# Optimization experiments

Measured on AMD Instinct MI355X. Metric: run time of the kernel, lower is better.

## Reference

```python
import jax, jax.numpy as jnp
import numpy as np

CODEBOOK_SIZE = 256
EMBED_DIM = 32
N_TOKENS = 524288
EPS = 1e-6


def l2norm(t, eps=EPS):
    # F.normalize(p=2): x / max(||x||, eps)
    n = jnp.sqrt(jnp.sum(t * t, axis=-1, keepdims=True))
    return t / jnp.maximum(n, eps)


def setup_inputs() -> dict:
    key = jax.random.key(0)
    kx, kw = jax.random.split(key)
    x = jax.random.normal(kx, (N_TOKENS, EMBED_DIM), dtype=jnp.float32)
    # embedding.weight.data.uniform_(-1/codebook_size, 1/codebook_size)
    codebook = jax.random.uniform(
        kw, (CODEBOOK_SIZE, EMBED_DIM), dtype=jnp.float32,
        minval=-1.0 / CODEBOOK_SIZE, maxval=1.0 / CODEBOOK_SIZE)
    return {"x": x, "codebook": codebook}


def reference(x, codebook):
    # --- find_nearest_codes: cdist + argmin + gather ---
    # squared euclidean distances have the same argmin as torch.cdist
    x2 = jnp.sum(x * x, axis=-1, keepdims=True)            # [N, 1]
    c2 = jnp.sum(codebook * codebook, axis=-1)             # [K]
    d2 = x2 - 2.0 * (x @ codebook.T) + c2[None, :]         # [N, K]
    indices = jnp.argmin(d2, axis=1)                       # [N] int
    quantized = codebook[indices]                          # [N, D]

    # --- update_usage: histogram over codes ---
    counts = jnp.zeros((CODEBOOK_SIZE,), dtype=jnp.float32).at[indices].add(1.0)

    # --- rotate_to(x, quantized): rotation-trick gradient estimator ---
    u = jax.lax.stop_gradient(l2norm(x))                   # detached direction of src
    q = jax.lax.stop_gradient(l2norm(quantized))           # detached direction of tgt
    w = jax.lax.stop_gradient(l2norm(u + q))               # Householder bisector, detached
    e = x                                                  # gradient flows through e only
    ew = jnp.sum(e * w, axis=-1, keepdims=True)            # (e @ w_col)
    eu = jnp.sum(e * u, axis=-1, keepdims=True)            # (e @ u_col)
    rotated = e - 2.0 * ew * w + 2.0 * eu * q              # [N, D]

    return rotated, indices, counts
```

## Files before the change

kernel.cpp:

```cpp
#include <hip/hip_runtime.h>

#define N_TOK   524288
#define KC      256
#define D       32
#define EPSF    1e-6f
#define TPT     64
#define NTILES  (N_TOK / TPT)
#define NBLK    768
#define BLKT    256

__global__ __launch_bounds__(BLKT) void vq_main(
    const float* __restrict__ x, const float* __restrict__ cb,
    float* __restrict__ out_rot, float* __restrict__ out_idx,
    float* __restrict__ ws_hist, float* __restrict__ out_cnt, int use_ws)
{
    __shared__ float ct[D][KC];
    __shared__ float c2s[KC];
    __shared__ float xt[D][TPT];
    __shared__ float x2s[TPT];
    __shared__ int   bidx[TPT];
    __shared__ float hist[KC];

    const int tid = threadIdx.x;

    {
#pragma clang fp contract(off)
        const float4* cb4 = (const float4*)(cb + (size_t)tid * D);
        float4 r[8];
#pragma unroll
        for (int j = 0; j < 8; j++) r[j] = cb4[j];
        float t[32];
#pragma unroll
        for (int j = 0; j < 8; j++) {
            t[4 * j + 0] = r[j].x * r[j].x;
            t[4 * j + 1] = r[j].y * r[j].y;
            t[4 * j + 2] = r[j].z * r[j].z;
            t[4 * j + 3] = r[j].w * r[j].w;
        }
        float pr[8];
#pragma unroll
        for (int j = 0; j < 8; j++)
            pr[j] = ((t[j] + t[j + 8]) + t[j + 16]) + t[j + 24];
        c2s[tid] = ((pr[0] + pr[1]) + (pr[2] + pr[3])) + ((pr[4] + pr[5]) + (pr[6] + pr[7]));
#pragma unroll
        for (int j = 0; j < 8; j++) {
            ct[4 * j + 0][tid] = r[j].x;
            ct[4 * j + 1][tid] = r[j].y;
            ct[4 * j + 2][tid] = r[j].z;
            ct[4 * j + 3][tid] = r[j].w;
        }
        hist[tid] = 0.f;
    }
    const int tt = tid >> 4;
    const int tc = tid & 15;
    __syncthreads();

    for (int tile = blockIdx.x; tile < NTILES; tile += gridDim.x) {
        const int tok0 = tile * TPT;

        {
            const float4* xg = (const float4*)(x + (size_t)tok0 * D + (size_t)tid * 8);
            float4 a = xg[0], b = xg[1];
            int tok = tid >> 2;
            int k0  = (tid & 3) * 8;
            xt[k0 + 0][tok] = a.x; xt[k0 + 1][tok] = a.y;
            xt[k0 + 2][tok] = a.z; xt[k0 + 3][tok] = a.w;
            xt[k0 + 4][tok] = b.x; xt[k0 + 5][tok] = b.y;
            xt[k0 + 6][tok] = b.z; xt[k0 + 7][tok] = b.w;
        }
        __syncthreads();

        if (tid < TPT) {
#pragma clang fp contract(off)
            float t[32];
#pragma unroll
            for (int k = 0; k < 32; k++) { float v = xt[k][tid]; t[k] = v * v; }
            float pr[8];
#pragma unroll
            for (int j = 0; j < 8; j++)
                pr[j] = ((t[j] + t[j + 8]) + t[j + 16]) + t[j + 24];
            x2s[tid] = ((pr[0] + pr[1]) + (pr[2] + pr[3])) + ((pr[4] + pr[5]) + (pr[6] + pr[7]));
        }
        __syncthreads();

        float x4[4];
#pragma unroll
        for (int i = 0; i < 4; i++) x4[i] = x2s[tt * 4 + i];

        float bestv[4] = {3.4e38f, 3.4e38f, 3.4e38f, 3.4e38f};
        int   besti[4] = {0x7fffffff, 0x7fffffff, 0x7fffffff, 0x7fffffff};
#pragma unroll
        for (int chunk = 0; chunk < 2; chunk++) {
            const int cbase = chunk * 128 + tc * 8;
            float acc[4][8];
#pragma unroll
            for (int i = 0; i < 4; i++)
#pragma unroll
                for (int j = 0; j < 8; j++) acc[i][j] = 0.f;

#pragma unroll 8
            for (int k = 0; k < D; k++) {
                const float4 xv = *(const float4*)&xt[k][tt * 4];
                const float4 c0 = *(const float4*)&ct[k][cbase];
                const float4 c1 = *(const float4*)&ct[k][cbase + 4];
                const float xs[4] = {xv.x, xv.y, xv.z, xv.w};
                const float cs[8] = {c0.x, c0.y, c0.z, c0.w, c1.x, c1.y, c1.z, c1.w};
#pragma unroll
                for (int i = 0; i < 4; i++)
#pragma unroll
                    for (int j = 0; j < 8; j++)
                        acc[i][j] = __builtin_fmaf(xs[i], cs[j], acc[i][j]);
            }
#pragma unroll
            for (int j = 0; j < 8; j++) {
                const float c2v = c2s[cbase + j];
#pragma unroll
                for (int i = 0; i < 4; i++) {
                    float t2 = x4[i] - 2.0f * acc[i][j];
                    float s  = t2 + c2v;
                    if (s < bestv[i]) { bestv[i] = s; besti[i] = cbase + j; }
                }
            }
        }
#pragma unroll
        for (int m = 1; m < 16; m <<= 1) {
#pragma unroll
            for (int i = 0; i < 4; i++) {
                float ov = __shfl_xor(bestv[i], m, 64);
                int   oi = __shfl_xor(besti[i], m, 64);
                if (ov < bestv[i] || (ov == bestv[i] && oi < besti[i])) {
                    bestv[i] = ov; besti[i] = oi;
                }
            }
        }
        if (tc == 0) {
#pragma unroll
            for (int i = 0; i < 4; i++) bidx[tt * 4 + i] = besti[i];
        }
        __syncthreads();

        {
            const int tok = tid >> 2;
            const int sub = tid & 3;
            const size_t gtok = (size_t)tok0 + tok;
            const float4* xg = (const float4*)(x + gtok * D + sub * 8);
            float4 xa = xg[0], xb = xg[1];
            const int bi = bidx[tok];
            const float4* cg = (const float4*)(cb + (size_t)bi * D + sub * 8);
            float4 ca = cg[0], cbv = cg[1];

            float xs8[8] = {xa.x, xa.y, xa.z, xa.w, xb.x, xb.y, xb.z, xb.w};
            float cs8[8] = {ca.x, ca.y, ca.z, ca.w, cbv.x, cbv.y, cbv.z, cbv.w};

            float px2 = 0.f, pc2 = 0.f;
#pragma unroll
            for (int j = 0; j < 8; j++) { px2 = fmaf(xs8[j], xs8[j], px2); pc2 = fmaf(cs8[j], cs8[j], pc2); }
            float x2 = px2 + __shfl_xor(px2, 1, 64); x2 += __shfl_xor(x2, 2, 64);
            float c2 = pc2 + __shfl_xor(pc2, 1, 64); c2 += __shfl_xor(c2, 2, 64);
            const float inx = 1.f / fmaxf(sqrtf(x2), EPSF);
            const float inc = 1.f / fmaxf(sqrtf(c2), EPSF);

            float us8[8], qs8[8], ws8[8];
            float pw2 = 0.f;
#pragma unroll
            for (int j = 0; j < 8; j++) {
                us8[j] = xs8[j] * inx;
                qs8[j] = cs8[j] * inc;
                ws8[j] = us8[j] + qs8[j];
                pw2 = fmaf(ws8[j], ws8[j], pw2);
            }
            float w2 = pw2 + __shfl_xor(pw2, 1, 64); w2 += __shfl_xor(w2, 2, 64);
            const float inw = 1.f / fmaxf(sqrtf(w2), EPSF);

            float pew = 0.f, peu = 0.f;
#pragma unroll
            for (int j = 0; j < 8; j++) {
                ws8[j] *= inw;
                pew = fmaf(xs8[j], ws8[j], pew);
                peu = fmaf(xs8[j], us8[j], peu);
            }
            float ew = pew + __shfl_xor(pew, 1, 64); ew += __shfl_xor(ew, 2, 64);
            float eu = peu + __shfl_xor(peu, 1, 64); eu += __shfl_xor(eu, 2, 64);

            float ro[8];
#pragma unroll
            for (int j = 0; j < 8; j++)
                ro[j] = xs8[j] - 2.f * ew * ws8[j] + 2.f * eu * qs8[j];

            float4* og = (float4*)(out_rot + gtok * D + sub * 8);
            og[0] = make_float4(ro[0], ro[1], ro[2], ro[3]);
            og[1] = make_float4(ro[4], ro[5], ro[6], ro[7]);

            if (sub == 0) {
                out_idx[gtok] = (float)bi;
                atomicAdd(&hist[bi], 1.f);
            }
        }
        __syncthreads();
    }

    if (use_ws) ws_hist[(size_t)blockIdx.x * KC + tid] = hist[tid];
    else        atomicAdd(&out_cnt[tid], hist[tid]);
}

__global__ __launch_bounds__(256) void vq_reduce(const float* __restrict__ ws,
                                                 float* __restrict__ out_cnt)
{
    const int c = blockIdx.x * 8 + (threadIdx.x >> 5);
    const int l = threadIdx.x & 31;
    float s = 0.f;
    for (int b = l; b < NBLK; b += 32) s += ws[(size_t)b * KC + c];
#pragma unroll
    for (int m = 1; m < 32; m <<= 1) s += __shfl_xor(s, m, 64);
    if (l == 0) out_cnt[c] = s;
}

extern "C" void kernel_launch(void* const* d_in, const int* in_sizes, int n_in,
                              void* d_out, int out_size, void* d_ws, size_t ws_size,
                              hipStream_t stream)
{
    const float* x  = (const float*)d_in[0];
    const float* cb = (const float*)d_in[1];
    float* out      = (float*)d_out;
    float* out_rot  = out;
    float* out_idx  = out + (size_t)N_TOK * D;
    float* out_cnt  = out_idx + N_TOK;

    const size_t ws_need = (size_t)NBLK * KC * sizeof(float);
    const int use_ws = (ws_size >= ws_need) ? 1 : 0;
    if (!use_ws) hipMemsetAsync(out_cnt, 0, KC * sizeof(float), stream);

    vq_main<<<NBLK, BLKT, 0, stream>>>(x, cb, out_rot, out_idx,
                                       (float*)d_ws, out_cnt, use_ws);
    if (use_ws) vq_reduce<<<32, 256, 0, stream>>>((const float*)d_ws, out_cnt);
}
```

Before: 242.1 us.

## Double-buffer token tiles, prefetch next tile, and keep x in registers

Prefetches the next tile's x into registers and stages it into a second shared buffer, so per-tile barriers drop from four to one. The squared norm of x is now computed with cross-lane shuffles during staging. The x values are reused from registers in the rotation phase instead of being reloaded from global memory. Best indices are passed by wave shuffle rather than through shared memory. It also computes all 16 codes per thread in one pass with an XOR-swizzled x layout, which raises register pressure in exchange for fewer LDS x reads and fewer barriers.

```diff
diff --git a/kernel.cpp b/kernel.cpp
--- a/kernel.cpp
+++ b/kernel.cpp
@@ -16,12 +16,12 @@
 {
     __shared__ float ct[D][KC];
     __shared__ float c2s[KC];
-    __shared__ float xt[D][TPT];
-    __shared__ float x2s[TPT];
-    __shared__ int   bidx[TPT];
+    __shared__ float xt[2][D][TPT];
+    __shared__ float x2s[2][TPT];
     __shared__ float hist[KC];
 
-    const int tid = threadIdx.x;
+    const int tid  = threadIdx.x;
+    const int lane = tid & 63;
 
     {
 #pragma clang fp contract(off)
@@ -51,77 +51,95 @@
         }
         hist[tid] = 0.f;
     }
-    const int tt = tid >> 4;
-    const int tc = tid & 15;
+
+    const int tt   = tid >> 4;
+    const int tc   = tid & 15;
+    const int tok  = tid >> 2;
+    const int sub  = tid & 3;
+    const int colw = tok ^ (sub << 4);
+
+    auto stage = [&](int buf, float4 a, float4 b) {
+#pragma clang fp contract(off)
+        float xs[8] = {a.x, a.y, a.z, a.w, b.x, b.y, b.z, b.w};
+        const int k0 = sub * 8;
+#pragma unroll
+        for (int j = 0; j < 8; j++) xt[buf][k0 + j][colw] = xs[j];
+        float sq[8];
+#pragma unroll
+        for (int j = 0; j < 8; j++) sq[j] = xs[j] * xs[j];
+        const int base = lane & ~3;
+        float pr[8];
+#pragma unroll
+        for (int j = 0; j < 8; j++) {
+            float t01 = sq[j] + __shfl_xor(sq[j], 1, 64);
+            float s2  = __shfl(sq[j], base + 2, 64);
+            float s3  = __shfl(sq[j], base + 3, 64);
+            pr[j] = (t01 + s2) + s3;
+        }
+        float v = ((pr[0] + pr[1]) + (pr[2] + pr[3])) + ((pr[4] + pr[5]) + (pr[6] + pr[7]));
+        if (sub == 0) x2s[buf][tok] = v;
+    };
+
+    float4 aC, bC;
+    {
+        const float4* xg = (const float4*)(x + (size_t)blockIdx.x * TPT * D + (size_t)tid * 8);
+        aC = xg[0]; bC = xg[1];
+    }
+    stage(0, aC, bC);
     __syncthreads();
 
+    int cur = 0;
     for (int tile = blockIdx.x; tile < NTILES; tile += gridDim.x) {
-        const int tok0 = tile * TPT;
-
-        {
-            const float4* xg = (const float4*)(x + (size_t)tok0 * D + (size_t)tid * 8);
-            float4 a = xg[0], b = xg[1];
-            int tok = tid >> 2;
-            int k0  = (tid & 3) * 8;
-            xt[k0 + 0][tok] = a.x; xt[k0 + 1][tok] = a.y;
-            xt[k0 + 2][tok] = a.z; xt[k0 + 3][tok] = a.w;
-            xt[k0 + 4][tok] = b.x; xt[k0 + 5][tok] = b.y;
-            xt[k0 + 6][tok] = b.z; xt[k0 + 7][tok] = b.w;
-        }
-        __syncthreads();
-
-        if (tid < TPT) {
-#pragma clang fp contract(off)
-            float t[32];
-#pragma unroll
-            for (int k = 0; k < 32; k++) { float v = xt[k][tid]; t[k] = v * v; }
-            float pr[8];
-#pragma unroll
-            for (int j = 0; j < 8; j++)
-                pr[j] = ((t[j] + t[j + 8]) + t[j + 16]) + t[j + 24];
-            x2s[tid] = ((pr[0] + pr[1]) + (pr[2] + pr[3])) + ((pr[4] + pr[5]) + (pr[6] + pr[7]));
-        }
-        __syncthreads();
+        const int nt = tile + gridDim.x;
+        const bool hasN = (nt < NTILES);
+        float4 aN = aC, bN = bC;
+        if (hasN) {
+            const float4* xg = (const float4*)(x + (size_t)nt * TPT * D + (size_t)tid * 8);
+            aN = xg[0]; bN = xg[1];
+        }
 
         float x4[4];
 #pragma unroll
-        for (int i = 0; i < 4; i++) x4[i] = x2s[tt * 4 + i];
+        for (int i = 0; i < 4; i++) x4[i] = x2s[cur][tt * 4 + i];
+
+        float acc[4][16];
+#pragma unroll
+        for (int i = 0; i < 4; i++)
+#pragma unroll
+            for (int j = 0; j < 16; j++) acc[i][j] = 0.f;
+
+#pragma unroll 4
+        for (int k = 0; k < D; k++) {
+            const int xcol = (tt * 4) ^ ((k >> 3) << 4);
+            const float4 xv = *(const float4*)&xt[cur][k][xcol];
+            const float4 v0 = *(const float4*)&ct[k][tc * 4];
+            const float4 v1 = *(const float4*)&ct[k][64 + tc * 4];
+            const float4 v2 = *(const float4*)&ct[k][128 + tc * 4];
+            const float4 v3 = *(const float4*)&ct[k][192 + tc * 4];
+            const float xs[4]  = {xv.x, xv.y, xv.z, xv.w};
+            const float cs[16] = {v0.x, v0.y, v0.z, v0.w, v1.x, v1.y, v1.z, v1.w,
+                                  v2.x, v2.y, v2.z, v2.w, v3.x, v3.y, v3.z, v3.w};
+#pragma unroll
+            for (int i = 0; i < 4; i++)
+#pragma unroll
+                for (int j = 0; j < 16; j++)
+                    acc[i][j] = __builtin_fmaf(xs[i], cs[j], acc[i][j]);
+        }
 
         float bestv[4] = {3.4e38f, 3.4e38f, 3.4e38f, 3.4e38f};
         int   besti[4] = {0x7fffffff, 0x7fffffff, 0x7fffffff, 0x7fffffff};
 #pragma unroll
-        for (int chunk = 0; chunk < 2; chunk++) {
-            const int cbase = chunk * 128 + tc * 8;
-            float acc[4][8];
-#pragma unroll
-            for (int i = 0; i < 4; i++)
-#pragma unroll
-                for (int j = 0; j < 8; j++) acc[i][j] = 0.f;
-
-#pragma unroll 8
-            for (int k = 0; k < D; k++) {
-                const float4 xv = *(const float4*)&xt[k][tt * 4];
-                const float4 c0 = *(const float4*)&ct[k][cbase];
-                const float4 c1 = *(const float4*)&ct[k][cbase + 4];
-                const float xs[4] = {xv.x, xv.y, xv.z, xv.w};
-                const float cs[8] = {c0.x, c0.y, c0.z, c0.w, c1.x, c1.y, c1.z, c1.w};
-#pragma unroll
-                for (int i = 0; i < 4; i++)
-#pragma unroll
-                    for (int j = 0; j < 8; j++)
-                        acc[i][j] = __builtin_fmaf(xs[i], cs[j], acc[i][j]);
-            }
-#pragma unroll
-            for (int j = 0; j < 8; j++) {
-                const float c2v = c2s[cbase + j];
-#pragma unroll
-                for (int i = 0; i < 4; i++) {
-                    float t2 = x4[i] - 2.0f * acc[i][j];
-                    float s  = t2 + c2v;
-                    if (s < bestv[i]) { bestv[i] = s; besti[i] = cbase + j; }
-                }
-            }
-        }
+        for (int j = 0; j < 16; j++) {
+            const int code = (j >> 2) * 64 + tc * 4 + (j & 3);
+            const float c2v = c2s[code];
+#pragma unroll
+            for (int i = 0; i < 4; i++) {
+                float t2 = x4[i] - 2.0f * acc[i][j];
+                float s  = t2 + c2v;
+                if (s < bestv[i]) { bestv[i] = s; besti[i] = code; }
+            }
+        }
+
 #pragma unroll
         for (int m = 1; m < 16; m <<= 1) {
 #pragma unroll
@@ -133,23 +151,21 @@
                 }
             }
         }
-        if (tc == 0) {
-#pragma unroll
-            for (int i = 0; i < 4; i++) bidx[tt * 4 + i] = besti[i];
-        }
-        __syncthreads();
+
+        const int src = lane & 48;
+        const int b0 = __shfl(besti[0], src, 64);
+        const int b1 = __shfl(besti[1], src, 64);
+        const int b2 = __shfl(besti[2], src, 64);
+        const int b3 = __shfl(besti[3], src, 64);
+        const int ii = (lane >> 2) & 3;
+        const int bi = (ii == 0) ? b0 : (ii == 1) ? b1 : (ii == 2) ? b2 : b3;
 
         {
-            const int tok = tid >> 2;
-            const int sub = tid & 3;
-            const size_t gtok = (size_t)tok0 + tok;
-            const float4* xg = (const float4*)(x + gtok * D + sub * 8);
-            float4 xa = xg[0], xb = xg[1];
-            const int bi = bidx[tok];
+            const size_t gtok = (size_t)tile * TPT + tok;
             const float4* cg = (const float4*)(cb + (size_t)bi * D + sub * 8);
             float4 ca = cg[0], cbv = cg[1];
 
-            float xs8[8] = {xa.x, xa.y, xa.z, xa.w, xb.x, xb.y, xb.z, xb.w};
+            float xs8[8] = {aC.x, aC.y, aC.z, aC.w, bC.x, bC.y, bC.z, bC.w};
             float cs8[8] = {ca.x, ca.y, ca.z, ca.w, cbv.x, cbv.y, cbv.z, cbv.w};
 
             float px2 = 0.f, pc2 = 0.f;
@@ -196,7 +212,10 @@
                 atomicAdd(&hist[bi], 1.f);
             }
         }
+
+        if (hasN) stage(cur ^ 1, aN, bN);
         __syncthreads();
+        aC = aN; bC = bN; cur ^= 1;
     }
 
     if (use_ws) ws_hist[(size_t)blockIdx.x * KC + tid] = hist[tid];
```

New measurement: 244.8 us. No clear change (+1.1%).

## Switch to one token per thread with codebook reads from global/scalar loads

Applied to the files above, without the earlier changes.

Replaces the shared-memory register-tiled 4x8 distance computation with a one-token-per-thread scheme. Each thread keeps its 32-element x row in registers and loops over all 256 codes, reading codebook rows directly from global memory through uniform, cache-resident loads. It also removes the persistent tile loop, launching one block per 256 tokens, and drops the shuffle reductions in the rotation epilogue. In exchange it loses the register-level reuse of the tiled GEMM, since each codebook element is now used once per load rather than across four tokens. Per-thread strided x loads of 128 bytes also coalesce less well.

```diff
diff --git a/kernel.cpp b/kernel.cpp
--- a/kernel.cpp
+++ b/kernel.cpp
@@ -4,21 +4,15 @@
 #define KC      256
 #define D       32
 #define EPSF    1e-6f
-#define TPT     64
-#define NTILES  (N_TOK / TPT)
-#define NBLK    768
+#define NBLK    2048
 #define BLKT    256
 
-__global__ __launch_bounds__(BLKT) void vq_main(
+__global__ __launch_bounds__(BLKT, 4) void vq_main(
     const float* __restrict__ x, const float* __restrict__ cb,
     float* __restrict__ out_rot, float* __restrict__ out_idx,
     float* __restrict__ ws_hist, float* __restrict__ out_cnt, int use_ws)
 {
-    __shared__ float ct[D][KC];
     __shared__ float c2s[KC];
-    __shared__ float xt[D][TPT];
-    __shared__ float x2s[TPT];
-    __shared__ int   bidx[TPT];
     __shared__ float hist[KC];
 
     const int tid = threadIdx.x;
@@ -42,162 +36,113 @@
         for (int j = 0; j < 8; j++)
             pr[j] = ((t[j] + t[j + 8]) + t[j + 16]) + t[j + 24];
         c2s[tid] = ((pr[0] + pr[1]) + (pr[2] + pr[3])) + ((pr[4] + pr[5]) + (pr[6] + pr[7]));
+        hist[tid] = 0.f;
+    }
+    __syncthreads();
+
+    const size_t tok = (size_t)blockIdx.x * BLKT + tid;
+
+    float xr[32];
+    {
+        const float4* xg = (const float4*)(x + tok * D);
 #pragma unroll
         for (int j = 0; j < 8; j++) {
-            ct[4 * j + 0][tid] = r[j].x;
-            ct[4 * j + 1][tid] = r[j].y;
-            ct[4 * j + 2][tid] = r[j].z;
-            ct[4 * j + 3][tid] = r[j].w;
+            float4 v = xg[j];
+            xr[4 * j + 0] = v.x; xr[4 * j + 1] = v.y;
+            xr[4 * j + 2] = v.z; xr[4 * j + 3] = v.w;
         }
-        hist[tid] = 0.f;
     }
-    const int tt = tid >> 4;
-    const int tc = tid & 15;
+
+    float x2v;
+    {
+#pragma clang fp contract(off)
+        float t[32];
+#pragma unroll
+        for (int k = 0; k < 32; k++) t[k] = xr[k] * xr[k];
+        float pr[8];
+#pragma unroll
+        for (int j = 0; j < 8; j++)
+            pr[j] = ((t[j] + t[j + 8]) + t[j + 16]) + t[j + 24];
+        x2v = ((pr[0] + pr[1]) + (pr[2] + pr[3])) + ((pr[4] + pr[5]) + (pr[6] + pr[7]));
+    }
+
+    float bestv = 3.4e38f;
+    int   besti = 0x7fffffff;
+#pragma unroll 2
+    for (int c = 0; c < KC; ++c) {
+        const float4* cr = (const float4*)(cb + (size_t)c * D);
+        const float4 q0 = cr[0], q1 = cr[1], q2 = cr[2], q3 = cr[3];
+        const float4 q4 = cr[4], q5 = cr[5], q6 = cr[6], q7 = cr[7];
+        const float cs[32] = {q0.x, q0.y, q0.z, q0.w, q1.x, q1.y, q1.z, q1.w,
+                              q2.x, q2.y, q2.z, q2.w, q3.x, q3.y, q3.z, q3.w,
+                              q4.x, q4.y, q4.z, q4.w, q5.x, q5.y, q5.z, q5.w,
+                              q6.x, q6.y, q6.z, q6.w, q7.x, q7.y, q7.z, q7.w};
+        float acc = 0.f;
+#pragma unroll
+        for (int k = 0; k < 32; ++k) acc = __builtin_fmaf(xr[k], cs[k], acc);
+        const float t2 = x2v - 2.0f * acc;
+        const float s  = t2 + c2s[c];
+        if (s < bestv) { bestv = s; besti = c; }
+    }
+
+    float cs[32];
+    {
+        const float4* cg = (const float4*)(cb + (size_t)besti * D);
+#pragma unroll
+        for (int j = 0; j < 8; j++) {
+            float4 v = cg[j];
+            cs[4 * j + 0] = v.x; cs[4 * j + 1] = v.y;
+            cs[4 * j + 2] = v.z; cs[4 * j + 3] = v.w;
+        }
+    }
+
+    float px2 = 0.f, pc2 = 0.f;
+#pragma unroll
+    for (int j = 0; j < 32; j++) {
+        px2 = fmaf(xr[j], xr[j], px2);
+        pc2 = fmaf(cs[j], cs[j], pc2);
+    }
+    const float inx = 1.f / fmaxf(sqrtf(px2), EPSF);
+    const float inc = 1.f / fmaxf(sqrtf(pc2), EPSF);
+
+    float pw2 = 0.f;
+#pragma unroll
+    for (int j = 0; j < 32; j++) {
+        const float wj = xr[j] * inx + cs[j] * inc;
+        pw2 = fmaf(wj, wj, pw2);
+    }
+    const float inw = 1.f / fmaxf(sqrtf(pw2), EPSF);
+
+    float pew = 0.f, peu = 0.f;
+#pragma unroll
+    for (int j = 0; j < 32; j++) {
+        const float uj = xr[j] * inx;
+        const float wj = (uj + cs[j] * inc) * inw;
+        pew = fmaf(xr[j], wj, pew);
+        peu = fmaf(xr[j], uj, peu);
+    }
+    const float ew = pew, eu = peu;
+
+    {
+        float4* og = (float4*)(out_rot + tok * D);
+#pragma unroll
+        for (int j = 0; j < 8; j++) {
+            float r4[4];
+#pragma unroll
+            for (int e = 0; e < 4; e++) {
+                const int jj = 4 * j + e;
+                const float uj = xr[jj] * inx;
+                const float wj = (uj + cs[jj] * inc) * inw;
+                const float qj = cs[jj] * inc;
+                r4[e] = xr[jj] - 2.f * ew * wj + 2.f * eu * qj;
+            }
+            og[j] = make_float4(r4[0], r4[1], r4[2], r4[3]);
+        }
+    }
+
+    out_idx[tok] = (float)besti;
+    atomicAdd(&hist[besti], 1.f);
     __syncthreads();
-
-    for (int tile = blockIdx.x; tile < NTILES; tile += gridDim.x) {
-        const int tok0 = tile * TPT;
-
-        {
-            const float4* xg = (const float4*)(x + (size_t)tok0 * D + (size_t)tid * 8);
-            float4 a = xg[0], b = xg[1];
-            int tok = tid >> 2;
-            int k0  = (tid & 3) * 8;
-            xt[k0 + 0][tok] = a.x; xt[k0 + 1][tok] = a.y;
-            xt[k0 + 2][tok] = a.z; xt[k0 + 3][tok] = a.w;
-            xt[k0 + 4][tok] = b.x; xt[k0 + 5][tok] = b.y;
-            xt[k0 + 6][tok] = b.z; xt[k0 + 7][tok] = b.w;
-        }
-        __syncthreads();
-
-        if (tid < TPT) {
-#pragma clang fp contract(off)
-            float t[32];
-#pragma unroll
-            for (int k = 0; k < 32; k++) { float v = xt[k][tid]; t[k] = v * v; }
-            float pr[8];
-#pragma unroll
-            for (int j = 0; j < 8; j++)
-                pr[j] = ((t[j] + t[j + 8]) + t[j + 16]) + t[j + 24];
-            x2s[tid] = ((pr[0] + pr[1]) + (pr[2] + pr[3])) + ((pr[4] + pr[5]) + (pr[6] + pr[7]));
-        }
-        __syncthreads();
-
-        float x4[4];
-#pragma unroll
-        for (int i = 0; i < 4; i++) x4[i] = x2s[tt * 4 + i];
-
-        float bestv[4] = {3.4e38f, 3.4e38f, 3.4e38f, 3.4e38f};
-        int   besti[4] = {0x7fffffff, 0x7fffffff, 0x7fffffff, 0x7fffffff};
-#pragma unroll
-        for (int chunk = 0; chunk < 2; chunk++) {
-            const int cbase = chunk * 128 + tc * 8;
-            float acc[4][8];
-#pragma unroll
-            for (int i = 0; i < 4; i++)
-#pragma unroll
-                for (int j = 0; j < 8; j++) acc[i][j] = 0.f;
-
-#pragma unroll 8
-            for (int k = 0; k < D; k++) {
-                const float4 xv = *(const float4*)&xt[k][tt * 4];
-                const float4 c0 = *(const float4*)&ct[k][cbase];
-                const float4 c1 = *(const float4*)&ct[k][cbase + 4];
-                const float xs[4] = {xv.x, xv.y, xv.z, xv.w};
-                const float cs[8] = {c0.x, c0.y, c0.z, c0.w, c1.x, c1.y, c1.z, c1.w};
-#pragma unroll
-                for (int i = 0; i < 4; i++)
-#pragma unroll
-                    for (int j = 0; j < 8; j++)
-                        acc[i][j] = __builtin_fmaf(xs[i], cs[j], acc[i][j]);
-            }
-#pragma unroll
-            for (int j = 0; j < 8; j++) {
-                const float c2v = c2s[cbase + j];
-#pragma unroll
-                for (int i = 0; i < 4; i++) {
-                    float t2 = x4[i] - 2.0f * acc[i][j];
-                    float s  = t2 + c2v;
-                    if (s < bestv[i]) { bestv[i] = s; besti[i] = cbase + j; }
-                }
-            }
-        }
-#pragma unroll
-        for (int m = 1; m < 16; m <<= 1) {
-#pragma unroll
-            for (int i = 0; i < 4; i++) {
-                float ov = __shfl_xor(bestv[i], m, 64);
-                int   oi = __shfl_xor(besti[i], m, 64);
-                if (ov < bestv[i] || (ov == bestv[i] && oi < besti[i])) {
-                    bestv[i] = ov; besti[i] = oi;
-                }
-            }
-        }
-        if (tc == 0) {
-#pragma unroll
-            for (int i = 0; i < 4; i++) bidx[tt * 4 + i] = besti[i];
-        }
-        __syncthreads();
-
-        {
-            const int tok = tid >> 2;
-            const int sub = tid & 3;
-            const size_t gtok = (size_t)tok0 + tok;
-            const float4* xg = (const float4*)(x + gtok * D + sub * 8);
-            float4 xa = xg[0], xb = xg[1];
-            const int bi = bidx[tok];
-            const float4* cg = (const float4*)(cb + (size_t)bi * D + sub * 8);
-            float4 ca = cg[0], cbv = cg[1];
-
-            float xs8[8] = {xa.x, xa.y, xa.z, xa.w, xb.x, xb.y, xb.z, xb.w};
-            float cs8[8] = {ca.x, ca.y, ca.z, ca.w, cbv.x, cbv.y, cbv.z, cbv.w};
-
-            float px2 = 0.f, pc2 = 0.f;
-#pragma unroll
-            for (int j = 0; j < 8; j++) { px2 = fmaf(xs8[j], xs8[j], px2); pc2 = fmaf(cs8[j], cs8[j], pc2); }
-            float x2 = px2 + __shfl_xor(px2, 1, 64); x2 += __shfl_xor(x2, 2, 64);
-            float c2 = pc2 + __shfl_xor(pc2, 1, 64); c2 += __shfl_xor(c2, 2, 64);
-            const float inx = 1.f / fmaxf(sqrtf(x2), EPSF);
-            const float inc = 1.f / fmaxf(sqrtf(c2), EPSF);
-
-            float us8[8], qs8[8], ws8[8];
-            float pw2 = 0.f;
-#pragma unroll
-            for (int j = 0; j < 8; j++) {
-                us8[j] = xs8[j] * inx;
-                qs8[j] = cs8[j] * inc;
-                ws8[j] = us8[j] + qs8[j];
-                pw2 = fmaf(ws8[j], ws8[j], pw2);
-            }
-            float w2 = pw2 + __shfl_xor(pw2, 1, 64); w2 += __shfl_xor(w2, 2, 64);
-            const float inw = 1.f / fmaxf(sqrtf(w2), EPSF);
-
-            float pew = 0.f, peu = 0.f;
-#pragma unroll
-            for (int j = 0; j < 8; j++) {
-                ws8[j] *= inw;
-                pew = fmaf(xs8[j], ws8[j], pew);
-                peu = fmaf(xs8[j], us8[j], peu);
-            }
-            float ew = pew + __shfl_xor(pew, 1, 64); ew += __shfl_xor(ew, 2, 64);
-            float eu = peu + __shfl_xor(peu, 1, 64); eu += __shfl_xor(eu, 2, 64);
-
-            float ro[8];
-#pragma unroll
-            for (int j = 0; j < 8; j++)
-                ro[j] = xs8[j] - 2.f * ew * ws8[j] + 2.f * eu * qs8[j];
-
-            float4* og = (float4*)(out_rot + gtok * D + sub * 8);
-            og[0] = make_float4(ro[0], ro[1], ro[2], ro[3]);
-            og[1] = make_float4(ro[4], ro[5], ro[6], ro[7]);
-
-            if (sub == 0) {
-                out_idx[gtok] = (float)bi;
-                atomicAdd(&hist[bi], 1.f);
-            }
-        }
-        __syncthreads();
-    }
 
     if (use_ws) ws_hist[(size_t)blockIdx.x * KC + tid] = hist[tid];
     else        atomicAdd(&out_cnt[tid], hist[tid]);
```

After: 281.5 us. 16.3% more time.

## Compute distances with split-bf16 MFMA and exact fp32 rescoring of near-ties

Applied to the files above, without the earlier changes.

Replaces the fp32 FMA distance GEMM with MFMA 16x16x32 bf16 instructions, splitting x and the codebook into hi/lo bf16 parts and using three MFMAs to approximate fp32 precision. Candidates within a margin of the per-token minimum are rescored in exact fp32 to keep the argmin matching the reference. Work is reorganized per wave (16-token strips) with no block-level barriers inside the loop, and the grid grows to 1024 blocks. The risks are divergent rescoring cost and argmin mismatches if the margin is too small.

```diff
diff --git a/kernel.cpp b/kernel.cpp
--- a/kernel.cpp
+++ b/kernel.cpp
@@ -4,24 +4,42 @@
 #define KC      256
 #define D       32
 #define EPSF    1e-6f
-#define TPT     64
-#define NTILES  (N_TOK / TPT)
-#define NBLK    768
+#define NBLK    1024
 #define BLKT    256
+#define NWAVES  (NBLK * 4)
+#define NSTRIP  (N_TOK / 16)
+#define SPW     (NSTRIP / NWAVES)
+#define MARGIN  1e-3f
+#define BIGF    3.4e38f
+
+typedef __attribute__((ext_vector_type(8))) short short8;
+typedef __attribute__((ext_vector_type(4))) float f32x4;
+
+__device__ __forceinline__ unsigned short f32_to_bf16_rne(float f) {
+    unsigned int u = __float_as_uint(f);
+    unsigned int r = u + 0x7fffu + ((u >> 16) & 1u);
+    return (unsigned short)(r >> 16);
+}
+__device__ __forceinline__ float bf16_to_f32(unsigned short h) {
+    return __uint_as_float(((unsigned int)h) << 16);
+}
 
 __global__ __launch_bounds__(BLKT) void vq_main(
     const float* __restrict__ x, const float* __restrict__ cb,
     float* __restrict__ out_rot, float* __restrict__ out_idx,
     float* __restrict__ ws_hist, float* __restrict__ out_cnt, int use_ws)
 {
-    __shared__ float ct[D][KC];
+    __shared__ unsigned int cbh[KC][20];
+    __shared__ unsigned int cbl[KC][20];
     __shared__ float c2s[KC];
-    __shared__ float xt[D][TPT];
-    __shared__ float x2s[TPT];
-    __shared__ int   bidx[TPT];
     __shared__ float hist[KC];
-
-    const int tid = threadIdx.x;
+    __shared__ float xs[4][16][36];
+    __shared__ float x2w[4][16];
+    __shared__ int   win[4][16];
+
+    const int tid  = threadIdx.x;
+    const int lane = tid & 63;
+    const int w    = tid >> 6;
 
     {
 #pragma clang fp contract(off)
@@ -29,125 +47,158 @@
         float4 r[8];
 #pragma unroll
         for (int j = 0; j < 8; j++) r[j] = cb4[j];
+        float v[32];
+#pragma unroll
+        for (int j = 0; j < 8; j++) {
+            v[4*j+0] = r[j].x; v[4*j+1] = r[j].y; v[4*j+2] = r[j].z; v[4*j+3] = r[j].w;
+        }
         float t[32];
 #pragma unroll
-        for (int j = 0; j < 8; j++) {
-            t[4 * j + 0] = r[j].x * r[j].x;
-            t[4 * j + 1] = r[j].y * r[j].y;
-            t[4 * j + 2] = r[j].z * r[j].z;
-            t[4 * j + 3] = r[j].w * r[j].w;
-        }
+        for (int k = 0; k < 32; k++) t[k] = v[k] * v[k];
         float pr[8];
 #pragma unroll
         for (int j = 0; j < 8; j++)
             pr[j] = ((t[j] + t[j + 8]) + t[j + 16]) + t[j + 24];
         c2s[tid] = ((pr[0] + pr[1]) + (pr[2] + pr[3])) + ((pr[4] + pr[5]) + (pr[6] + pr[7]));
-#pragma unroll
-        for (int j = 0; j < 8; j++) {
-            ct[4 * j + 0][tid] = r[j].x;
-            ct[4 * j + 1][tid] = r[j].y;
-            ct[4 * j + 2][tid] = r[j].z;
-            ct[4 * j + 3][tid] = r[j].w;
+
+        unsigned int hp[16], lp[16];
+#pragma unroll
+        for (int q = 0; q < 16; q++) { hp[q] = 0u; lp[q] = 0u; }
+#pragma unroll
+        for (int j = 0; j < 32; j++) {
+            unsigned short h = f32_to_bf16_rne(v[j]);
+            float lo = v[j] - bf16_to_f32(h);
+            unsigned short l = f32_to_bf16_rne(lo);
+            hp[j >> 1] |= ((unsigned int)h) << (16 * (j & 1));
+            lp[j >> 1] |= ((unsigned int)l) << (16 * (j & 1));
+        }
+#pragma unroll
+        for (int q = 0; q < 4; q++) {
+            ((uint4*)&cbh[tid][0])[q] = make_uint4(hp[4*q], hp[4*q+1], hp[4*q+2], hp[4*q+3]);
+            ((uint4*)&cbl[tid][0])[q] = make_uint4(lp[4*q], lp[4*q+1], lp[4*q+2], lp[4*q+3]);
         }
         hist[tid] = 0.f;
     }
-    const int tt = tid >> 4;
-    const int tc = tid & 15;
     __syncthreads();
 
-    for (int tile = blockIdx.x; tile < NTILES; tile += gridDim.x) {
-        const int tok0 = tile * TPT;
-
+    const int col = lane & 15;
+    const int kc  = lane >> 4;
+
+    float c2r[16];
+#pragma unroll
+    for (int t = 0; t < 16; t++) c2r[t] = c2s[t * 16 + col];
+
+    const int gw = blockIdx.x * 4 + w;
+
+    for (int s = 0; s < SPW; ++s) {
+        const int strip = gw + NWAVES * s;
+        const int tb    = strip * 16;
+
+        const float* xp = x + (size_t)(tb + col) * D + kc * 8;
+        const float4 f0 = *(const float4*)xp;
+        const float4 f1 = *(const float4*)(xp + 4);
+        *(float4*)&xs[w][col][kc * 8]     = f0;
+        *(float4*)&xs[w][col][kc * 8 + 4] = f1;
+
+        short8 ah, al;
         {
-            const float4* xg = (const float4*)(x + (size_t)tok0 * D + (size_t)tid * 8);
-            float4 a = xg[0], b = xg[1];
-            int tok = tid >> 2;
-            int k0  = (tid & 3) * 8;
-            xt[k0 + 0][tok] = a.x; xt[k0 + 1][tok] = a.y;
-            xt[k0 + 2][tok] = a.z; xt[k0 + 3][tok] = a.w;
-            xt[k0 + 4][tok] = b.x; xt[k0 + 5][tok] = b.y;
-            xt[k0 + 6][tok] = b.z; xt[k0 + 7][tok] = b.w;
-        }
-        __syncthreads();
-
-        if (tid < TPT) {
+            float xf[8] = {f0.x, f0.y, f0.z, f0.w, f1.x, f1.y, f1.z, f1.w};
+#pragma unroll
+            for (int j = 0; j < 8; j++) {
+                unsigned short h = f32_to_bf16_rne(xf[j]);
+                float lo = xf[j] - bf16_to_f32(h);
+                ah[j] = (short)h;
+                al[j] = (short)f32_to_bf16_rne(lo);
+            }
+        }
+
+        {
 #pragma clang fp contract(off)
-            float t[32];
-#pragma unroll
-            for (int k = 0; k < 32; k++) { float v = xt[k][tid]; t[k] = v * v; }
+            const int tok4 = lane >> 2, sub = lane & 3, base = lane & ~3;
+            const float4 a = *(const float4*)&xs[w][tok4][sub * 8];
+            const float4 b = *(const float4*)&xs[w][tok4][sub * 8 + 4];
+            float sq[8] = {a.x*a.x, a.y*a.y, a.z*a.z, a.w*a.w,
+                           b.x*b.x, b.y*b.y, b.z*b.z, b.w*b.w};
             float pr[8];
 #pragma unroll
-            for (int j = 0; j < 8; j++)
-                pr[j] = ((t[j] + t[j + 8]) + t[j + 16]) + t[j + 24];
-            x2s[tid] = ((pr[0] + pr[1]) + (pr[2] + pr[3])) + ((pr[4] + pr[5]) + (pr[6] + pr[7]));
-        }
-        __syncthreads();
-
-        float x4[4];
-#pragma unroll
-        for (int i = 0; i < 4; i++) x4[i] = x2s[tt * 4 + i];
-
-        float bestv[4] = {3.4e38f, 3.4e38f, 3.4e38f, 3.4e38f};
-        int   besti[4] = {0x7fffffff, 0x7fffffff, 0x7fffffff, 0x7fffffff};
-#pragma unroll
-        for (int chunk = 0; chunk < 2; chunk++) {
-            const int cbase = chunk * 128 + tc * 8;
-            float acc[4][8];
-#pragma unroll
-            for (int i = 0; i < 4; i++)
-#pragma unroll
-                for (int j = 0; j < 8; j++) acc[i][j] = 0.f;
-
-#pragma unroll 8
-            for (int k = 0; k < D; k++) {
-                const float4 xv = *(const float4*)&xt[k][tt * 4];
-                const float4 c0 = *(const float4*)&ct[k][cbase];
-                const float4 c1 = *(const float4*)&ct[k][cbase + 4];
-                const float xs[4] = {xv.x, xv.y, xv.z, xv.w};
-                const float cs[8] = {c0.x, c0.y, c0.z, c0.w, c1.x, c1.y, c1.z, c1.w};
-#pragma unroll
-                for (int i = 0; i < 4; i++)
-#pragma unroll
-                    for (int j = 0; j < 8; j++)
-                        acc[i][j] = __builtin_fmaf(xs[i], cs[j], acc[i][j]);
-            }
-#pragma unroll
-            for (int j = 0; j < 8; j++) {
-                const float c2v = c2s[cbase + j];
-#pragma unroll
-                for (int i = 0; i < 4; i++) {
-                    float t2 = x4[i] - 2.0f * acc[i][j];
-                    float s  = t2 + c2v;
-                    if (s < bestv[i]) { bestv[i] = s; besti[i] = cbase + j; }
+            for (int j = 0; j < 8; j++) {
+                float t01 = sq[j] + __shfl_xor(sq[j], 1, 64);
+                float s2  = __shfl(sq[j], base + 2, 64);
+                float s3  = __shfl(sq[j], base + 3, 64);
+                pr[j] = (t01 + s2) + s3;
+            }
+            float v = ((pr[0]+pr[1]) + (pr[2]+pr[3])) + ((pr[4]+pr[5]) + (pr[6]+pr[7]));
+            if (sub == 0) x2w[w][tok4] = v;
+        }
+
+        float sarr[16][4];
+        float mn[4] = {BIGF, BIGF, BIGF, BIGF};
+#pragma unroll
+        for (int t = 0; t < 16; ++t) {
+            const int code = t * 16 + col;
+            const short8 bh = *(const short8*)&cbh[code][kc * 4];
+            const short8 bl = *(const short8*)&cbl[code][kc * 4];
+            f32x4 acc = {0.f, 0.f, 0.f, 0.f};
+            acc = __builtin_amdgcn_mfma_f32_16x16x32_bf16(al, bh, acc, 0, 0, 0);
+            acc = __builtin_amdgcn_mfma_f32_16x16x32_bf16(ah, bl, acc, 0, 0, 0);
+            acc = __builtin_amdgcn_mfma_f32_16x16x32_bf16(ah, bh, acc, 0, 0, 0);
+#pragma unroll
+            for (int r = 0; r < 4; ++r) {
+                const float sv = __builtin_fmaf(-2.f, acc[r], c2r[t]);
+                sarr[t][r] = sv;
+                mn[r] = fminf(mn[r], sv);
+            }
+        }
+#pragma unroll
+        for (int m = 1; m < 16; m <<= 1)
+#pragma unroll
+            for (int r = 0; r < 4; ++r)
+                mn[r] = fminf(mn[r], __shfl_xor(mn[r], m, 64));
+
+        float bE[4] = {BIGF, BIGF, BIGF, BIGF};
+        int   bI[4] = {0x7fffffff, 0x7fffffff, 0x7fffffff, 0x7fffffff};
+#pragma unroll
+        for (int t = 0; t < 16; ++t)
+#pragma unroll
+            for (int r = 0; r < 4; ++r)
+                if (sarr[t][r] <= mn[r] + MARGIN) {
+                    const int code = t * 16 + col;
+                    const int trow = kc * 4 + r;
+                    const float* crow = cb + (size_t)code * D;
+                    float acc = 0.f;
+#pragma unroll
+                    for (int q = 0; q < 8; ++q) {
+                        const float4 xq = *(const float4*)&xs[w][trow][q * 4];
+                        const float4 cq = *(const float4*)&crow[q * 4];
+                        acc = __builtin_fmaf(xq.x, cq.x, acc);
+                        acc = __builtin_fmaf(xq.y, cq.y, acc);
+                        acc = __builtin_fmaf(xq.z, cq.z, acc);
+                        acc = __builtin_fmaf(xq.w, cq.w, acc);
+                    }
+                    const float t2 = x2w[w][trow] - 2.0f * acc;
+                    const float d  = t2 + c2s[code];
+                    if (d < bE[r] || (d == bE[r] && code < bI[r])) { bE[r] = d; bI[r] = code; }
                 }
-            }
-        }
-#pragma unroll
-        for (int m = 1; m < 16; m <<= 1) {
-#pragma unroll
-            for (int i = 0; i < 4; i++) {
-                float ov = __shfl_xor(bestv[i], m, 64);
-                int   oi = __shfl_xor(besti[i], m, 64);
-                if (ov < bestv[i] || (ov == bestv[i] && oi < besti[i])) {
-                    bestv[i] = ov; besti[i] = oi;
-                }
-            }
-        }
-        if (tc == 0) {
-#pragma unroll
-            for (int i = 0; i < 4; i++) bidx[tt * 4 + i] = besti[i];
-        }
-        __syncthreads();
+#pragma unroll
+        for (int m = 1; m < 16; m <<= 1)
+#pragma unroll
+            for (int r = 0; r < 4; ++r) {
+                const float ov = __shfl_xor(bE[r], m, 64);
+                const int   oi = __shfl_xor(bI[r], m, 64);
+                if (ov < bE[r] || (ov == bE[r] && oi < bI[r])) { bE[r] = ov; bI[r] = oi; }
+            }
+        if (col == 0)
+#pragma unroll
+            for (int r = 0; r < 4; ++r) win[w][kc * 4 + r] = bI[r];
 
         {
-            const int tok = tid >> 2;
-            const int sub = tid & 3;
-            const size_t gtok = (size_t)tok0 + tok;
-            const float4* xg = (const float4*)(x + gtok * D + sub * 8);
-            float4 xa = xg[0], xb = xg[1];
-            const int bi = bidx[tok];
+            const int tok = lane >> 2, sub = lane & 3;
+            const size_t gtok = (size_t)tb + tok;
+            const int bi = win[w][tok];
             const float4* cg = (const float4*)(cb + (size_t)bi * D + sub * 8);
-            float4 ca = cg[0], cbv = cg[1];
+            const float4 ca = cg[0], cbv = cg[1];
+            const float4 xa = *(const float4*)&xs[w][tok][sub * 8];
+            const float4 xb = *(const float4*)&xs[w][tok][sub * 8 + 4];
 
             float xs8[8] = {xa.x, xa.y, xa.z, xa.w, xb.x, xb.y, xb.z, xb.w};
             float cs8[8] = {ca.x, ca.y, ca.z, ca.w, cbv.x, cbv.y, cbv.z, cbv.w};
@@ -196,9 +247,9 @@
                 atomicAdd(&hist[bi], 1.f);
             }
         }
-        __syncthreads();
     }
 
+    __syncthreads();
     if (use_ws) ws_hist[(size_t)blockIdx.x * KC + tid] = hist[tid];
     else        atomicAdd(&out_cnt[tid], hist[tid]);
 }
```

Result: slower. 522.3 us (+115.8%).
